# Optimization experiments

Hardware: AMD Instinct MI355X
Metric: run time of the kernel (lower is better)

## Reference

```python
import jax, jax.numpy as jnp
import numpy as np

# RSM hyperparameters (match init_kwargs)
M, N, K = 1000, 4, 25          # columns, cells per column, column winners
TC = M * N                      # total cells
GAMMA, EPS, MEM_GAIN = 0.5, 0.5, 1.0


def topk_mask(x, k):
    """Binary mask of top-k entries along last axis (x: [B, M])."""
    _, idx = jax.lax.top_k(x, k)
    rows = jnp.arange(x.shape[0])[:, None]
    return jnp.zeros_like(x).at[rows, idx].set(1.0)


def rsm_step(carry, x_t, w_a, w_b, w_d, b_d):
    x_b, phi, psi = carry                      # each [B, TC]
    # Feedforward (column-level) and lateral (cell-level) drive
    z_a = x_t @ w_a.T                          # [B, M]
    z_b = MEM_GAIN * (x_b @ w_b.T)             # [B, TC]
    sigma = jnp.repeat(z_a, N, axis=-1) + z_b  # broadcast cols to cells, [B, TC]
    # Inhibition (rsm_inhibition boost strategy)
    pi = sigma * (1.0 - phi)                   # [B, TC]
    pi_c = pi.reshape(-1, M, N)
    lam = pi_c.max(-1)                         # column max, [B, M]
    m_pi = topk_mask(lam, K)                   # k winning columns, [B, M]
    # one winning cell per column (k_winner_cells=1)
    m_lam = jax.nn.one_hot(jnp.argmax(pi_c, -1), N, dtype=pi.dtype)  # [B, M, N]
    mask = jax.lax.stop_gradient((m_pi[..., None] * m_lam).reshape(-1, TC))
    y = jnp.tanh(mask * sigma)                 # sparse activation, [B, TC]
    # Memory trace (eps decay) and inhibition trace (gamma decay)
    psi_new = jnp.maximum(psi * EPS, y)
    phi_new = jnp.maximum(phi * GAMMA, y)
    x_b_new = psi_new                          # x_b_norm=False
    # Decode from column-level activity (decode_from_full_memory=False)
    y_col = y.reshape(-1, M, N).max(-1)        # [B, M]
    out = y_col @ w_d.T + b_d                  # [B, d_out]
    return (x_b_new, phi_new, psi_new), out


def setup_inputs() -> dict:
    key = jax.random.key(0)
    ks = jax.random.split(key, 5)
    T, B, D_IN, D_OUT = 64, 128, 1024, 1024
    sd = 0.03  # init std from _init_linear_weights
    return {
        "x": jax.random.normal(ks[0], (T, B, D_IN), dtype=jnp.float32),
        "w_a": sd * jax.random.normal(ks[1], (M, D_IN), dtype=jnp.float32),
        "w_b": sd * jax.random.normal(ks[2], (TC, TC), dtype=jnp.float32),
        "w_d": sd * jax.random.normal(ks[3], (D_OUT, M), dtype=jnp.float32),
        "b_d": sd * jax.random.normal(ks[4], (D_OUT,), dtype=jnp.float32),
    }


def reference(x, w_a, w_b, w_d, b_d):
    T, B = x.shape[0], x.shape[1]
    init = (jnp.zeros((B, TC), x.dtype),  # x_b (memory)
            jnp.zeros((B, TC), x.dtype),  # phi (inhibition)
            jnp.zeros((B, TC), x.dtype))  # psi (trace)
    step = lambda c, xt: rsm_step(c, xt, w_a, w_b, w_d, b_d)
    _, outs = jax.lax.scan(step, init, x)
    return outs  # [T, B, d_out]
```

## Files before the change

kernel.cpp:

```cpp
#include <hip/hip_runtime.h>
#include <hip/hip_bf16.h>
#include <math.h>

#define MCOL   1000
#define NCELL  4
#define TCELL  4000
#define KWIN   25
#define TT     64
#define BB     128
#define DIN    1024
#define DOUT   1024

__global__ void transpose_k(const float* __restrict__ src, float* __restrict__ dst,
                            int R, int C) {
    __shared__ float tile[32][33];
    int c0 = blockIdx.x * 32, r0 = blockIdx.y * 32;
    int tx = threadIdx.x, ty = threadIdx.y;
#pragma unroll
    for (int q = 0; q < 4; ++q) {
        int r = r0 + ty + q * 8, c = c0 + tx;
        tile[ty + q * 8][tx] = (r < R && c < C) ? src[(size_t)r * C + c] : 0.f;
    }
    __syncthreads();
#pragma unroll
    for (int q = 0; q < 4; ++q) {
        int c = c0 + ty + q * 8, r = r0 + tx;
        if (c < C && r < R) dst[(size_t)c * R + r] = tile[tx][ty + q * 8];
    }
}

__launch_bounds__(256, 2)
__global__ void za_gemm(const float* __restrict__ A,
                        const float* __restrict__ Bw,
                        float* __restrict__ C) {
    __shared__ float As[16][132];
    __shared__ float Bs[16][132];
    const int i0 = blockIdx.x * 128;
    const int m0 = blockIdx.y * 128;
    const int tid = threadIdx.x;
    const int tx = tid & 15, ty = tid >> 4;
    float acc[8][8];
#pragma unroll
    for (int a = 0; a < 8; ++a)
#pragma unroll
        for (int b = 0; b < 8; ++b) acc[a][b] = 0.f;

    for (int k0 = 0; k0 < DIN; k0 += 16) {
#pragma unroll
        for (int p = 0; p < 2; ++p) {
            int f = tid + p * 256;
            int row = f >> 2, c4 = (f & 3) * 4;
            float4 v = *reinterpret_cast<const float4*>(
                &A[(size_t)(i0 + row) * DIN + k0 + c4]);
            As[c4 + 0][row] = v.x; As[c4 + 1][row] = v.y;
            As[c4 + 2][row] = v.z; As[c4 + 3][row] = v.w;
            int m = m0 + row;
            float4 w = make_float4(0.f, 0.f, 0.f, 0.f);
            if (m < MCOL)
                w = *reinterpret_cast<const float4*>(&Bw[(size_t)m * DIN + k0 + c4]);
            Bs[c4 + 0][row] = w.x; Bs[c4 + 1][row] = w.y;
            Bs[c4 + 2][row] = w.z; Bs[c4 + 3][row] = w.w;
        }
        __syncthreads();
#pragma unroll
        for (int kk = 0; kk < 16; ++kk) {
            float4 a0 = *reinterpret_cast<const float4*>(&As[kk][ty * 8]);
            float4 a1 = *reinterpret_cast<const float4*>(&As[kk][ty * 8 + 4]);
            float4 b0 = *reinterpret_cast<const float4*>(&Bs[kk][tx * 8]);
            float4 b1 = *reinterpret_cast<const float4*>(&Bs[kk][tx * 8 + 4]);
            float av[8] = {a0.x, a0.y, a0.z, a0.w, a1.x, a1.y, a1.z, a1.w};
            float bv[8] = {b0.x, b0.y, b0.z, b0.w, b1.x, b1.y, b1.z, b1.w};
#pragma unroll
            for (int ii = 0; ii < 8; ++ii)
#pragma unroll
                for (int jj = 0; jj < 8; ++jj)
                    acc[ii][jj] = fmaf(av[ii], bv[jj], acc[ii][jj]);
        }
        __syncthreads();
    }
#pragma unroll
    for (int ii = 0; ii < 8; ++ii) {
        int i = i0 + ty * 8 + ii;
#pragma unroll
        for (int jj = 0; jj < 8; ++jj) {
            int m = m0 + tx * 8 + jj;
            if (m < MCOL) C[(size_t)i * MCOL + m] = acc[ii][jj];
        }
    }
}

__launch_bounds__(1024, 1)
__global__ void rsm_kernel(const float* __restrict__ ZA,
                           const float* __restrict__ wbT,
                           const float* __restrict__ wdT,
                           const float* __restrict__ bd,
                           float* __restrict__ out) {
    const int b = blockIdx.x;
    const int tid = threadIdx.x;
    const int lane = tid & 63, wid = tid >> 6;
    const bool colOwner = (tid < MCOL);

    __shared__ int   hist[16][256];
    __shared__ int   htot[256];
    __shared__ int   winflag[1024];
    __shared__ int   wscan[16];
    __shared__ int   wscan2[16];
    __shared__ int   bc[8];
    __shared__ unsigned int candU[1024];
    __shared__ int   candI[1024];
    __shared__ int   wcellS[KWIN];
    __shared__ int   wcolS[KWIN];
    __shared__ float wdeltaS[KWIN];
    __shared__ float wycolS[KWIN];

    float Z4[4]   = {0.f, 0.f, 0.f, 0.f};
    float phi4[4] = {0.f, 0.f, 0.f, 0.f};
    float psi4[4] = {0.f, 0.f, 0.f, 0.f};
    const float breg = bd[tid];

    for (int t = 0; t < TT; ++t) {
        float sig[4] = {0.f, 0.f, 0.f, 0.f};
        float lam = -INFINITY;
        int argn = 0;
        if (colOwner) {
            float za = ZA[(size_t)(t * BB + b) * MCOL + tid];
#pragma unroll
            for (int n = 0; n < 4; ++n) {
                sig[n] = za + Z4[n];
                float pi = sig[n] * (1.0f - phi4[n]);
                if (pi > lam) { lam = pi; argn = n; }
            }
        }
        unsigned int ubits = __float_as_uint(lam);
        unsigned int u = (ubits & 0x80000000u) ? ~ubits : (ubits | 0x80000000u);

        int need = KWIN;
        int active = 1;
#pragma unroll
        for (int lev = 0; lev < 2; ++lev) {
            int mybyte = (lev == 0) ? (int)(u >> 24) : (int)((u >> 16) & 255u);
#pragma unroll
            for (int i = 0; i < 4; ++i) ((int*)hist)[tid + i * 1024] = 0;
            if (lev == 0) {
                winflag[tid] = 0;
                if (tid < 8) bc[tid] = 0;
            }
            __syncthreads();
            if (active) atomicAdd(&hist[wid][mybyte], 1);
            __syncthreads();
            if (tid < 256) {
                int s = 0;
#pragma unroll
                for (int w = 0; w < 16; ++w) s += hist[w][tid];
                htot[tid] = s;
            }
            __syncthreads();
            if (wid == 0) {
                int h0 = htot[lane * 4 + 0], h1 = htot[lane * 4 + 1];
                int h2 = htot[lane * 4 + 2], h3 = htot[lane * 4 + 3];
                int s = h0 + h1 + h2 + h3;
                int p = s;
                for (int d = 1; d < 64; d <<= 1) {
                    int q = __shfl_up(p, d);
                    if (lane >= d) p += q;
                }
                int T_all = __shfl(p, 63);
                int pexc = p - s;
                int X = T_all - need;
                int pr0 = pexc, pr1 = pexc + h0, pr2 = pexc + h0 + h1,
                    pr3 = pexc + h0 + h1 + h2;
                int lb = -1;
                if (pr0 <= X) lb = lane * 4 + 0;
                if (pr1 <= X) lb = lane * 4 + 1;
                if (pr2 <= X) lb = lane * 4 + 2;
                if (pr3 <= X) lb = lane * 4 + 3;
                int bmax = lb;
                for (int d = 32; d; d >>= 1) bmax = max(bmax, __shfl_xor(bmax, d));
                if (lb == bmax && lb >= 0) {
                    int k3 = bmax & 3;
                    int prb = (k3 == 0) ? pr0 : (k3 == 1) ? pr1 : (k3 == 2) ? pr2 : pr3;
                    int hb  = (k3 == 0) ? h0  : (k3 == 1) ? h1  : (k3 == 2) ? h2  : h3;
                    bc[0] = bmax;
                    bc[1] = T_all - prb - hb;
                }
            }
            __syncthreads();
            int bstar = bc[0], above = bc[1];
            int wasActive = active;
            if (wasActive && mybyte > bstar) winflag[tid] = 1;
            active = wasActive && (mybyte == bstar);
            need -= above;
        }
        if (active) {
            int s = atomicAdd(&bc[2], 1);
            candU[s] = u;
            candI[s] = tid;
        }
        __syncthreads();
        int c2 = bc[2];
        if (c2 == need) {
            if (active) winflag[tid] = 1;
        } else if (tid == 0) {
            for (int s = 0; s < need; ++s) {
                unsigned int bu = 0u; int bi = 0; int bj = -1;
                for (int j = 0; j < c2; ++j) {
                    int ci = candI[j];
                    if (ci < 0) continue;
                    unsigned int cu = candU[j];
                    if (bj < 0 || cu > bu || (cu == bu && ci < bi)) {
                        bu = cu; bi = ci; bj = j;
                    }
                }
                winflag[bi] = 1;
                candI[bj] = -1;
            }
        }
        __syncthreads();

        int wf = winflag[tid];
        unsigned long long ball = __ballot(wf != 0);
        int myrank = __popcll(ball & ((1ull << lane) - 1ull));
        if (lane == 0) wscan[wid] = __popcll(ball);
        __syncthreads();
        if (tid < 16) {
            int s = 0;
            for (int w = 0; w < tid; ++w) s += wscan[w];
            wscan2[tid] = s;
        }
        __syncthreads();

        if (colOwner) {
            float y = 0.f;
            if (wf) {
                y = tanhf(sig[argn]);
                int slot = wscan2[wid] + myrank;
                float pdec = 0.5f * psi4[argn];
                float pnew = fmaxf(pdec, y);
                wcellS[slot]  = tid * 4 + argn;
                wcolS[slot]   = tid;
                wdeltaS[slot] = pnew - pdec;
                wycolS[slot]  = fmaxf(y, 0.f);
            }
#pragma unroll
            for (int n = 0; n < 4; ++n) {
                float yn = (wf && n == argn) ? y : 0.f;
                psi4[n] = fmaxf(0.5f * psi4[n], yn);
                phi4[n] = fmaxf(0.5f * phi4[n], yn);
                Z4[n] *= 0.5f;
            }
        }
        __syncthreads();

        if (colOwner) {
            float a0 = 0.f, a1 = 0.f, a2 = 0.f, a3 = 0.f;
#pragma unroll 5
            for (int j = 0; j < KWIN; ++j) {
                float d = wdeltaS[j];
                if (d != 0.f) {
                    const float4 w4 = *reinterpret_cast<const float4*>(
                        &wbT[(size_t)wcellS[j] * TCELL + tid * 4]);
                    a0 = fmaf(d, w4.x, a0);
                    a1 = fmaf(d, w4.y, a1);
                    a2 = fmaf(d, w4.z, a2);
                    a3 = fmaf(d, w4.w, a3);
                }
            }
            Z4[0] += a0; Z4[1] += a1; Z4[2] += a2; Z4[3] += a3;
        }

        {
            float s = 0.f;
#pragma unroll 5
            for (int j = 0; j < KWIN; ++j) {
                float yc = wycolS[j];
                if (yc != 0.f)
                    s = fmaf(yc, wdT[(size_t)wcolS[j] * DOUT + tid], s);
            }
            out[(size_t)(t * BB + b) * DOUT + tid] = s + breg;
        }
    }
}

extern "C" void kernel_launch(void* const* d_in, const int* in_sizes, int n_in,
                              void* d_out, int out_size, void* d_ws, size_t ws_size,
                              hipStream_t stream) {
    const float* x   = (const float*)d_in[0];
    const float* w_a = (const float*)d_in[1];
    const float* w_b = (const float*)d_in[2];
    const float* w_d = (const float*)d_in[3];
    const float* b_d = (const float*)d_in[4];
    float* out = (float*)d_out;

    const size_t need_bytes = (size_t)(16000000 + 1024000 + 8192000) * 4;
    if (ws_size < need_bytes) return;
    float* wbT = (float*)d_ws;
    float* wdT = wbT + 16000000;
    float* ZA  = wdT + 1024000;

    transpose_k<<<dim3(125, 125), dim3(32, 8), 0, stream>>>(w_b, wbT, TCELL, TCELL);
    transpose_k<<<dim3(32, 32),  dim3(32, 8), 0, stream>>>(w_d, wdT, DOUT, MCOL);
    za_gemm<<<dim3(64, 8), 256, 0, stream>>>(x, w_a, ZA);
    rsm_kernel<<<128, 1024, 0, stream>>>(ZA, wbT, wdT, b_d, out);
}
```

Before: 1.775 ms.

## Halve block size with two columns per thread and batched weight gathers

The recurrent kernel now runs 512 threads per batch row, each owning two columns, so there are fewer waves per barrier and cheaper histogram reductions. Tie-breaking among candidates at the threshold is done by parallel rank counting instead of a serial thread-0 loop. Winners are recorded directly with an atomic slot counter, and the prefix scan over ballots is gone. The w_b and w_d gathers are unrolled into register arrays with no zero-skip, giving more memory parallelism per thread. This raises register pressure and relies on exactly 25 winners being written every step.

```diff
diff --git a/kernel.cpp b/kernel.cpp
--- a/kernel.cpp
+++ b/kernel.cpp
@@ -89,7 +89,7 @@
     }
 }
 
-__launch_bounds__(1024, 1)
+__launch_bounds__(512, 2)
 __global__ void rsm_kernel(const float* __restrict__ ZA,
                            const float* __restrict__ wbT,
                            const float* __restrict__ wdT,
@@ -98,186 +98,245 @@
     const int b = blockIdx.x;
     const int tid = threadIdx.x;
     const int lane = tid & 63, wid = tid >> 6;
-    const bool colOwner = (tid < MCOL);
-
-    __shared__ int   hist[16][256];
-    __shared__ int   htot[256];
-    __shared__ int   winflag[1024];
-    __shared__ int   wscan[16];
-    __shared__ int   wscan2[16];
-    __shared__ int   bc[8];
+    const bool hasB = (tid < (MCOL - 512));
+    const int c0 = tid, c1 = tid + 512;
+
+    __shared__ int   hist0[8][256];
+    __shared__ int   hist1[8][256];
+    __shared__ int   sel[8];
     __shared__ unsigned int candU[1024];
     __shared__ int   candI[1024];
-    __shared__ int   wcellS[KWIN];
-    __shared__ int   wcolS[KWIN];
-    __shared__ float wdeltaS[KWIN];
-    __shared__ float wycolS[KWIN];
-
-    float Z4[4]   = {0.f, 0.f, 0.f, 0.f};
-    float phi4[4] = {0.f, 0.f, 0.f, 0.f};
-    float psi4[4] = {0.f, 0.f, 0.f, 0.f};
-    const float breg = bd[tid];
+    __shared__ int   wcellS[28];
+    __shared__ float wdeltaS[28];
+    __shared__ int   wcolS[28];
+    __shared__ float wycolS[28];
+
+    float Za[4] = {0,0,0,0}, Zb[4] = {0,0,0,0};
+    float pha[4] = {0,0,0,0}, phb[4] = {0,0,0,0};
+    float psa[4] = {0,0,0,0}, psb[4] = {0,0,0,0};
+    const float breg0 = bd[tid], breg1 = bd[tid + 512];
 
     for (int t = 0; t < TT; ++t) {
-        float sig[4] = {0.f, 0.f, 0.f, 0.f};
-        float lam = -INFINITY;
-        int argn = 0;
-        if (colOwner) {
-            float za = ZA[(size_t)(t * BB + b) * MCOL + tid];
-#pragma unroll
-            for (int n = 0; n < 4; ++n) {
-                sig[n] = za + Z4[n];
-                float pi = sig[n] * (1.0f - phi4[n]);
-                if (pi > lam) { lam = pi; argn = n; }
-            }
-        }
-        unsigned int ubits = __float_as_uint(lam);
-        unsigned int u = (ubits & 0x80000000u) ? ~ubits : (ubits | 0x80000000u);
-
-        int need = KWIN;
-        int active = 1;
-#pragma unroll
-        for (int lev = 0; lev < 2; ++lev) {
-            int mybyte = (lev == 0) ? (int)(u >> 24) : (int)((u >> 16) & 255u);
-#pragma unroll
-            for (int i = 0; i < 4; ++i) ((int*)hist)[tid + i * 1024] = 0;
-            if (lev == 0) {
-                winflag[tid] = 0;
-                if (tid < 8) bc[tid] = 0;
-            }
-            __syncthreads();
-            if (active) atomicAdd(&hist[wid][mybyte], 1);
-            __syncthreads();
-            if (tid < 256) {
-                int s = 0;
-#pragma unroll
-                for (int w = 0; w < 16; ++w) s += hist[w][tid];
-                htot[tid] = s;
-            }
-            __syncthreads();
-            if (wid == 0) {
-                int h0 = htot[lane * 4 + 0], h1 = htot[lane * 4 + 1];
-                int h2 = htot[lane * 4 + 2], h3 = htot[lane * 4 + 3];
-                int s = h0 + h1 + h2 + h3;
-                int p = s;
-                for (int d = 1; d < 64; d <<= 1) {
-                    int q = __shfl_up(p, d);
-                    if (lane >= d) p += q;
-                }
-                int T_all = __shfl(p, 63);
-                int pexc = p - s;
-                int X = T_all - need;
-                int pr0 = pexc, pr1 = pexc + h0, pr2 = pexc + h0 + h1,
-                    pr3 = pexc + h0 + h1 + h2;
-                int lb = -1;
-                if (pr0 <= X) lb = lane * 4 + 0;
-                if (pr1 <= X) lb = lane * 4 + 1;
-                if (pr2 <= X) lb = lane * 4 + 2;
-                if (pr3 <= X) lb = lane * 4 + 3;
-                int bmax = lb;
-                for (int d = 32; d; d >>= 1) bmax = max(bmax, __shfl_xor(bmax, d));
-                if (lb == bmax && lb >= 0) {
-                    int k3 = bmax & 3;
-                    int prb = (k3 == 0) ? pr0 : (k3 == 1) ? pr1 : (k3 == 2) ? pr2 : pr3;
-                    int hb  = (k3 == 0) ? h0  : (k3 == 1) ? h1  : (k3 == 2) ? h2  : h3;
-                    bc[0] = bmax;
-                    bc[1] = T_all - prb - hb;
-                }
-            }
-            __syncthreads();
-            int bstar = bc[0], above = bc[1];
-            int wasActive = active;
-            if (wasActive && mybyte > bstar) winflag[tid] = 1;
-            active = wasActive && (mybyte == bstar);
-            need -= above;
-        }
-        if (active) {
-            int s = atomicAdd(&bc[2], 1);
-            candU[s] = u;
-            candI[s] = tid;
-        }
-        __syncthreads();
-        int c2 = bc[2];
-        if (c2 == need) {
-            if (active) winflag[tid] = 1;
-        } else if (tid == 0) {
-            for (int s = 0; s < need; ++s) {
-                unsigned int bu = 0u; int bi = 0; int bj = -1;
-                for (int j = 0; j < c2; ++j) {
-                    int ci = candI[j];
-                    if (ci < 0) continue;
-                    unsigned int cu = candU[j];
-                    if (bj < 0 || cu > bu || (cu == bu && ci < bi)) {
-                        bu = cu; bi = ci; bj = j;
-                    }
-                }
-                winflag[bi] = 1;
-                candI[bj] = -1;
-            }
-        }
-        __syncthreads();
-
-        int wf = winflag[tid];
-        unsigned long long ball = __ballot(wf != 0);
-        int myrank = __popcll(ball & ((1ull << lane) - 1ull));
-        if (lane == 0) wscan[wid] = __popcll(ball);
-        __syncthreads();
-        if (tid < 16) {
-            int s = 0;
-            for (int w = 0; w < tid; ++w) s += wscan[w];
-            wscan2[tid] = s;
-        }
-        __syncthreads();
-
-        if (colOwner) {
-            float y = 0.f;
-            if (wf) {
-                y = tanhf(sig[argn]);
-                int slot = wscan2[wid] + myrank;
-                float pdec = 0.5f * psi4[argn];
-                float pnew = fmaxf(pdec, y);
-                wcellS[slot]  = tid * 4 + argn;
-                wcolS[slot]   = tid;
-                wdeltaS[slot] = pnew - pdec;
-                wycolS[slot]  = fmaxf(y, 0.f);
-            }
-#pragma unroll
-            for (int n = 0; n < 4; ++n) {
-                float yn = (wf && n == argn) ? y : 0.f;
-                psi4[n] = fmaxf(0.5f * psi4[n], yn);
-                phi4[n] = fmaxf(0.5f * phi4[n], yn);
-                Z4[n] *= 0.5f;
-            }
-        }
-        __syncthreads();
-
-        if (colOwner) {
-            float a0 = 0.f, a1 = 0.f, a2 = 0.f, a3 = 0.f;
-#pragma unroll 5
-            for (int j = 0; j < KWIN; ++j) {
-                float d = wdeltaS[j];
-                if (d != 0.f) {
-                    const float4 w4 = *reinterpret_cast<const float4*>(
-                        &wbT[(size_t)wcellS[j] * TCELL + tid * 4]);
-                    a0 = fmaf(d, w4.x, a0);
-                    a1 = fmaf(d, w4.y, a1);
-                    a2 = fmaf(d, w4.z, a2);
-                    a3 = fmaf(d, w4.w, a3);
-                }
-            }
-            Z4[0] += a0; Z4[1] += a1; Z4[2] += a2; Z4[3] += a3;
-        }
-
-        {
-            float s = 0.f;
-#pragma unroll 5
-            for (int j = 0; j < KWIN; ++j) {
-                float yc = wycolS[j];
-                if (yc != 0.f)
-                    s = fmaf(yc, wdT[(size_t)wcolS[j] * DOUT + tid], s);
-            }
-            out[(size_t)(t * BB + b) * DOUT + tid] = s + breg;
-        }
+        const float* zaRow = ZA + (size_t)(t * BB + b) * MCOL;
+        float za0 = zaRow[c0];
+        float za1 = hasB ? zaRow[c1] : 0.f;
+
+        float sig0[4], sig1[4];
+        float lam0 = -INFINITY, lam1 = -INFINITY;
+        int an0 = 0, an1 = 0;
+#pragma unroll
+        for (int n = 0; n < 4; ++n) {
+            sig0[n] = za0 + Za[n];
+            float pi = sig0[n] * (1.0f - pha[n]);
+            if (pi > lam0) { lam0 = pi; an0 = n; }
+            sig1[n] = za1 + Zb[n];
+            float pi1 = sig1[n] * (1.0f - phb[n]);
+            if (pi1 > lam1) { lam1 = pi1; an1 = n; }
+        }
+        unsigned int ub0 = __float_as_uint(lam0);
+        unsigned int u0 = (ub0 & 0x80000000u) ? ~ub0 : (ub0 | 0x80000000u);
+        unsigned int ub1 = __float_as_uint(hasB ? lam1 : -INFINITY);
+        unsigned int u1 = (ub1 & 0x80000000u) ? ~ub1 : (ub1 | 0x80000000u);
+
+#pragma unroll
+        for (int i = 0; i < 4; ++i) {
+            ((int*)hist0)[tid + i * 512] = 0;
+            ((int*)hist1)[tid + i * 512] = 0;
+        }
+        if (tid < 8) sel[tid] = 0;
+        __syncthreads();
+
+        float ysave0 = 0.f, ysave1 = 0.f;
+        auto record0 = [&]() {
+            int slot = atomicAdd(&sel[5], 1);
+            float y = tanhf(sig0[an0]);
+            float pdec = 0.5f * psa[an0];
+            wcellS[slot]  = c0 * 4 + an0;
+            wdeltaS[slot] = fmaxf(pdec, y) - pdec;
+            wcolS[slot]   = c0;
+            wycolS[slot]  = fmaxf(y, 0.f);
+            ysave0 = y;
+        };
+        auto record1 = [&]() {
+            int slot = atomicAdd(&sel[5], 1);
+            float y = tanhf(sig1[an1]);
+            float pdec = 0.5f * psb[an1];
+            wcellS[slot]  = c1 * 4 + an1;
+            wdeltaS[slot] = fmaxf(pdec, y) - pdec;
+            wcolS[slot]   = c1;
+            wycolS[slot]  = fmaxf(y, 0.f);
+            ysave1 = y;
+        };
+
+        atomicAdd(&hist0[wid][u0 >> 24], 1);
+        if (hasB) atomicAdd(&hist0[wid][u1 >> 24], 1);
+        __syncthreads();
+        if (wid == 0) {
+            int h0 = 0, h1 = 0, h2 = 0, h3 = 0;
+#pragma unroll
+            for (int w = 0; w < 8; ++w) {
+                h0 += hist0[w][lane * 4 + 0]; h1 += hist0[w][lane * 4 + 1];
+                h2 += hist0[w][lane * 4 + 2]; h3 += hist0[w][lane * 4 + 3];
+            }
+            int s = h0 + h1 + h2 + h3;
+            int p = s;
+            for (int d = 1; d < 64; d <<= 1) {
+                int q = __shfl_up(p, d);
+                if (lane >= d) p += q;
+            }
+            int T_all = __shfl(p, 63);
+            int pexc = p - s;
+            int X = T_all - KWIN;
+            int pr1 = pexc + h0, pr2 = pr1 + h1, pr3 = pr2 + h2;
+            int lb = -1;
+            if (pexc <= X) lb = lane * 4 + 0;
+            if (pr1  <= X) lb = lane * 4 + 1;
+            if (pr2  <= X) lb = lane * 4 + 2;
+            if (pr3  <= X) lb = lane * 4 + 3;
+            int bmax = lb;
+            for (int d = 32; d; d >>= 1) bmax = max(bmax, __shfl_xor(bmax, d));
+            if (lb == bmax && lb >= 0) {
+                int k3 = bmax & 3;
+                int prb = (k3 == 0) ? pexc : (k3 == 1) ? pr1 : (k3 == 2) ? pr2 : pr3;
+                int hb  = (k3 == 0) ? h0   : (k3 == 1) ? h1  : (k3 == 2) ? h2  : h3;
+                sel[0] = bmax;
+                sel[1] = T_all - prb - hb;
+            }
+        }
+        __syncthreads();
+        const int bstar0 = sel[0];
+        const int byte00 = (int)(u0 >> 24), byte01 = (int)(u1 >> 24);
+        const int act0 = (byte00 == bstar0);
+        const int act1 = hasB && (byte01 == bstar0);
+        if (byte00 > bstar0) record0();
+        if (hasB && byte01 > bstar0) record1();
+
+        if (act0) atomicAdd(&hist1[wid][(u0 >> 16) & 255u], 1);
+        if (act1) atomicAdd(&hist1[wid][(u1 >> 16) & 255u], 1);
+        __syncthreads();
+        if (wid == 0) {
+            int need1 = KWIN - sel[1];
+            int h0 = 0, h1 = 0, h2 = 0, h3 = 0;
+#pragma unroll
+            for (int w = 0; w < 8; ++w) {
+                h0 += hist1[w][lane * 4 + 0]; h1 += hist1[w][lane * 4 + 1];
+                h2 += hist1[w][lane * 4 + 2]; h3 += hist1[w][lane * 4 + 3];
+            }
+            int s = h0 + h1 + h2 + h3;
+            int p = s;
+            for (int d = 1; d < 64; d <<= 1) {
+                int q = __shfl_up(p, d);
+                if (lane >= d) p += q;
+            }
+            int T_all = __shfl(p, 63);
+            int pexc = p - s;
+            int X = T_all - need1;
+            int pr1 = pexc + h0, pr2 = pr1 + h1, pr3 = pr2 + h2;
+            int lb = -1;
+            if (pexc <= X) lb = lane * 4 + 0;
+            if (pr1  <= X) lb = lane * 4 + 1;
+            if (pr2  <= X) lb = lane * 4 + 2;
+            if (pr3  <= X) lb = lane * 4 + 3;
+            int bmax = lb;
+            for (int d = 32; d; d >>= 1) bmax = max(bmax, __shfl_xor(bmax, d));
+            if (lb == bmax && lb >= 0) {
+                int k3 = bmax & 3;
+                int prb = (k3 == 0) ? pexc : (k3 == 1) ? pr1 : (k3 == 2) ? pr2 : pr3;
+                int hb  = (k3 == 0) ? h0   : (k3 == 1) ? h1  : (k3 == 2) ? h2  : h3;
+                sel[2] = bmax;
+                sel[3] = T_all - prb - hb;
+            }
+        }
+        __syncthreads();
+        const int bstar1 = sel[2];
+        const int need2 = (KWIN - sel[1]) - sel[3];
+        const int byte10 = (int)((u0 >> 16) & 255u), byte11 = (int)((u1 >> 16) & 255u);
+        const int a0b = act0 && (byte10 == bstar1);
+        const int a1b = act1 && (byte11 == bstar1);
+        if (act0 && byte10 > bstar1) record0();
+        if (act1 && byte11 > bstar1) record1();
+        if (a0b) { int s = atomicAdd(&sel[4], 1); candU[s] = u0; candI[s] = c0; }
+        if (a1b) { int s = atomicAdd(&sel[4], 1); candU[s] = u1; candI[s] = c1; }
+        __syncthreads();
+        const int c2 = sel[4];
+        if (a0b) {
+            int rank = 0;
+            for (int j = 0; j < c2; ++j) {
+                unsigned int cu = candU[j]; int ci = candI[j];
+                rank += (cu > u0) || (cu == u0 && ci < c0);
+            }
+            if (rank < need2) record0();
+        }
+        if (a1b) {
+            int rank = 0;
+            for (int j = 0; j < c2; ++j) {
+                unsigned int cu = candU[j]; int ci = candI[j];
+                rank += (cu > u1) || (cu == u1 && ci < c1);
+            }
+            if (rank < need2) record1();
+        }
+#pragma unroll
+        for (int n = 0; n < 4; ++n) {
+            float yn0 = (n == an0) ? ysave0 : 0.f;
+            psa[n] = fmaxf(0.5f * psa[n], yn0);
+            pha[n] = fmaxf(0.5f * pha[n], yn0);
+            Za[n] *= 0.5f;
+            float yn1 = (n == an1) ? ysave1 : 0.f;
+            psb[n] = fmaxf(0.5f * psb[n], yn1);
+            phb[n] = fmaxf(0.5f * phb[n], yn1);
+            Zb[n] *= 0.5f;
+        }
+        __syncthreads();
+
+        float4 ga0[13], gb0[13];
+#pragma unroll
+        for (int j = 0; j < 13; ++j) {
+            const float* p = wbT + (size_t)wcellS[j] * TCELL;
+            ga0[j] = *reinterpret_cast<const float4*>(p + 4 * c0);
+            gb0[j] = hasB ? *reinterpret_cast<const float4*>(p + 4 * c1)
+                          : make_float4(0.f, 0.f, 0.f, 0.f);
+        }
+        float dv0[KWIN], dv1[KWIN];
+#pragma unroll
+        for (int j = 0; j < KWIN; ++j) {
+            const float* q = wdT + (size_t)wcolS[j] * DOUT;
+            dv0[j] = q[tid];
+            dv1[j] = q[tid + 512];
+        }
+#pragma unroll
+        for (int j = 0; j < 13; ++j) {
+            float d = wdeltaS[j];
+            Za[0] = fmaf(d, ga0[j].x, Za[0]); Za[1] = fmaf(d, ga0[j].y, Za[1]);
+            Za[2] = fmaf(d, ga0[j].z, Za[2]); Za[3] = fmaf(d, ga0[j].w, Za[3]);
+            Zb[0] = fmaf(d, gb0[j].x, Zb[0]); Zb[1] = fmaf(d, gb0[j].y, Zb[1]);
+            Zb[2] = fmaf(d, gb0[j].z, Zb[2]); Zb[3] = fmaf(d, gb0[j].w, Zb[3]);
+        }
+        float4 ga1[12], gb1[12];
+#pragma unroll
+        for (int j = 0; j < 12; ++j) {
+            const float* p = wbT + (size_t)wcellS[13 + j] * TCELL;
+            ga1[j] = *reinterpret_cast<const float4*>(p + 4 * c0);
+            gb1[j] = hasB ? *reinterpret_cast<const float4*>(p + 4 * c1)
+                          : make_float4(0.f, 0.f, 0.f, 0.f);
+        }
+        float s0 = breg0, s1 = breg1;
+#pragma unroll
+        for (int j = 0; j < KWIN; ++j) {
+            float yc = wycolS[j];
+            s0 = fmaf(yc, dv0[j], s0);
+            s1 = fmaf(yc, dv1[j], s1);
+        }
+#pragma unroll
+        for (int j = 0; j < 12; ++j) {
+            float d = wdeltaS[13 + j];
+            Za[0] = fmaf(d, ga1[j].x, Za[0]); Za[1] = fmaf(d, ga1[j].y, Za[1]);
+            Za[2] = fmaf(d, ga1[j].z, Za[2]); Za[3] = fmaf(d, ga1[j].w, Za[3]);
+            Zb[0] = fmaf(d, gb1[j].x, Zb[0]); Zb[1] = fmaf(d, gb1[j].y, Zb[1]);
+            Zb[2] = fmaf(d, gb1[j].z, Zb[2]); Zb[3] = fmaf(d, gb1[j].w, Zb[3]);
+        }
+        float* orow = out + (size_t)(t * BB + b) * DOUT;
+        orow[tid] = s0;
+        orow[tid + 512] = s1;
     }
 }
 
@@ -300,5 +359,5 @@
     transpose_k<<<dim3(125, 125), dim3(32, 8), 0, stream>>>(w_b, wbT, TCELL, TCELL);
     transpose_k<<<dim3(32, 32),  dim3(32, 8), 0, stream>>>(w_d, wdT, DOUT, MCOL);
     za_gemm<<<dim3(64, 8), 256, 0, stream>>>(x, w_a, ZA);
-    rsm_kernel<<<128, 1024, 0, stream>>>(ZA, wbT, wdT, b_d, out);
+    rsm_kernel<<<128, 512, 0, stream>>>(ZA, wbT, wdT, b_d, out);
 }
```

Measured after the change: 2.299 ms. 29.5% more time.
